# Kernel tuning notes

Measured on AMD Instinct MI355X. Metric: run time of the kernel, lower is better.

## Reference

```python
import jax, jax.numpy as jnp
import numpy as np

B, N, D, D1, R, O = 256, 32, 128, 128, 8, 8


def setup_inputs() -> dict:
    key = jax.random.key(0)
    k = jax.random.split(key, 7)
    return {
        "center_h": jax.random.normal(k[0], (B, D), dtype=jnp.float32),
        "raw_neighbors": jax.random.normal(k[1], (B, N, D), dtype=jnp.float32),
        "M": jax.random.normal(k[2], (R, O, D, D1), dtype=jnp.float32) * 0.05,
        "b": jax.random.normal(k[3], (R, O, D1), dtype=jnp.float32) * 0.01,
        "center_o": jax.random.randint(k[4], (B,), 0, O, dtype=jnp.int32),
        "s_types": jax.random.randint(k[5], (B, N), 0, R, dtype=jnp.int32),
        "o_types": jax.random.randint(k[6], (B, N), 0, O, dtype=jnp.int32),
    }


def reference(center_h, raw_neighbors, M, b, center_o, s_types, o_types):
    # --- center projection: for each example b, all relations r, with o = center_o[b]
    M_center = M[:, center_o]                      # [R, B, D, D1]
    b_center = b[:, center_o]                      # [R, B, D1]
    h_center = jnp.einsum('bd,rbdj->brj', center_h, M_center)  # [B, R, D1]
    h_center = h_center + jnp.transpose(b_center, (1, 0, 2))

    # --- neighbor projection: per-(example, neighbor) (s_type, o_type)-indexed matrix
    s_idx = jnp.maximum(s_types, 0)
    o_idx = jnp.maximum(o_types, 0)
    M_neighbor = M[s_idx, o_idx]                   # [B, N, D, D1] (large gather)
    h_neighbor = jnp.einsum('bnd,bndj->bnj', raw_neighbors, M_neighbor)  # [B, N, D1]
    h_neighbor = h_neighbor + b[s_idx, o_idx]

    # tf.nn.gelu default is exact (erf-based)
    return (jax.nn.gelu(h_center, approximate=False),
            jax.nn.gelu(h_neighbor, approximate=False))
```

## Files before the change

kernel.cpp:

```cpp
#include <hip/hip_runtime.h>
#include <math.h>

#define NPAIR 64
#define NCENTER 2048
#define WCAP 48
#define RSLOT 32

typedef __attribute__((ext_vector_type(8))) short bfrag8;
typedef __attribute__((ext_vector_type(8))) unsigned short u16x8;
typedef __attribute__((ext_vector_type(4))) float f32x4;

__device__ __forceinline__ float gelu_f(float v) {
    return 0.5f * v * (1.0f + erff(v * 0.70710678118654752f));
}
__device__ __forceinline__ unsigned short f2bf(float f) {
    unsigned int u = __float_as_uint(f);
    return (unsigned short)((u + 0x7FFFu + ((u >> 16) & 1u)) >> 16);
}

__global__ __launch_bounds__(256) void fused_kernel(
    const float* __restrict__ center_h,
    const float* __restrict__ raw_neighbors,
    const float* __restrict__ Mg,
    const float* __restrict__ bias,
    const int* __restrict__ center_o,
    const int* __restrict__ s_types,
    const int* __restrict__ o_types,
    float* __restrict__ out)
{
    __shared__ __align__(16) unsigned short Mbt[128 * 128];
    __shared__ __align__(16) unsigned short Xs[RSLOT * 128];
    __shared__ int list[4 * WCAP];
    __shared__ int cnts[4];
    __shared__ int rowid[RSLOT];

    const int t    = threadIdx.x;
    const int wave = t >> 6, lane = t & 63;
    const int pair = blockIdx.x & 63, slice = blockIdx.x >> 6;
    const int r0 = pair >> 3, o0 = pair & 7;

    const int4 svv = ((const int4*)s_types)[slice * 256 + t];
    const int4 ovv = ((const int4*)o_types)[slice * 256 + t];
    const int my_b  = slice * 32 + wave * 8 + (lane & 7);
    const int my_co = center_o[my_b];

    {
        const int dblk = t >> 4, cblk = t & 15;
        const float* bp = Mg + pair * 16384 + dblk * 8 * 128 + cblk * 8;
        float gg[8][8];
        #pragma unroll
        for (int r = 0; r < 8; ++r) {
            const float4 x0 = *(const float4*)(bp + r * 128);
            const float4 x1 = *(const float4*)(bp + r * 128 + 4);
            gg[r][0] = x0.x; gg[r][1] = x0.y; gg[r][2] = x0.z; gg[r][3] = x0.w;
            gg[r][4] = x1.x; gg[r][5] = x1.y; gg[r][6] = x1.z; gg[r][7] = x1.w;
        }
        #pragma unroll
        for (int i = 0; i < 8; ++i) {
            u16x8 w;
            #pragma unroll
            for (int j = 0; j < 8; ++j) w[j] = f2bf(gg[j][i]);
            const int c  = cblk * 8 + i;
            const int sl = (dblk ^ (cblk & 7) ^ i) << 4;
            *(u16x8*)((char*)Mbt + c * 256 + sl) = w;
        }
    }

    int cw = 0;
    {
        const bool match = (lane < 8) && (my_co == o0);
        const unsigned long long mk = __ballot(match);
        const int pre = __builtin_amdgcn_mbcnt_hi(
            (unsigned)(mk >> 32), __builtin_amdgcn_mbcnt_lo((unsigned)mk, 0));
        if (match) {
            const int pos = cw + pre;
            if (pos < WCAP) list[wave * WCAP + pos] = my_b * 8 + r0;
        }
        cw += __popcll(mk);
    }
    {
        const int ss[4] = { svv.x, svv.y, svv.z, svv.w };
        const int oo[4] = { ovv.x, ovv.y, ovv.z, ovv.w };
        const int base_nid = slice * 1024 + t * 4;
        #pragma unroll
        for (int j = 0; j < 4; ++j) {
            const int s = ss[j] < 0 ? 0 : ss[j];
            const int o = oo[j] < 0 ? 0 : oo[j];
            const bool match = (s == r0) & (o == o0);
            const unsigned long long mk = __ballot(match);
            const int pre = __builtin_amdgcn_mbcnt_hi(
                (unsigned)(mk >> 32), __builtin_amdgcn_mbcnt_lo((unsigned)mk, 0));
            if (match) {
                const int pos = cw + pre;
                if (pos < WCAP) list[wave * WCAP + pos] = NCENTER + base_nid + j;
            }
            cw += __popcll(mk);
            if (cw > WCAP) cw = WCAP;
        }
    }
    if (lane == 0) cnts[wave] = cw;
    __syncthreads();

    const int c0_ = cnts[0], c1_ = cnts[1], c2_ = cnts[2];
    const int cnt = c0_ + c1_ + c2_ + cnts[3];

    const int lo16 = lane & 15, hi4 = lane >> 4;
    const int cA = wave * 32 + lo16;
    const int cB = cA + 16;
    const float bvA = bias[pair * 128 + cA];
    const float bvB = bias[pair * 128 + cB];
    const int keyA = ((cA >> 3) & 7) ^ (cA & 7);
    const int keyB = ((cB >> 3) & 7) ^ (cB & 7);
    const int rsw  = lo16 & 7;

    for (int base = 0; base < cnt; base += RSLOT) {
        const int csz = (cnt - base < RSLOT) ? (cnt - base) : RSLOT;

        if (t < RSLOT) {
            int id = -1;
            int a = base + t;
            if (a < cnt) {
                int sw = 0;
                if (a >= c0_) { a -= c0_; sw = 1;
                    if (a >= c1_) { a -= c1_; sw = 2;
                        if (a >= c2_) { a -= c2_; sw = 3; } } }
                id = list[sw * WCAP + a];
            }
            rowid[t] = id;
        }
        __syncthreads();

        #pragma unroll
        for (int i = 0; i < 2; ++i) {
            const int flat = i * 256 + t;
            const int row = flat >> 4, ch = flat & 15;
            const int id = rowid[row];
            u16x8 w = {0, 0, 0, 0, 0, 0, 0, 0};
            if (id >= 0) {
                const float* xp = (id < NCENTER) ? center_h + (id >> 3) * 128
                                                 : raw_neighbors + (id - NCENTER) * 128;
                const float4 x0 = *(const float4*)(xp + ch * 8);
                const float4 x1 = *(const float4*)(xp + ch * 8 + 4);
                w[0] = f2bf(x0.x); w[1] = f2bf(x0.y); w[2] = f2bf(x0.z); w[3] = f2bf(x0.w);
                w[4] = f2bf(x1.x); w[5] = f2bf(x1.y); w[6] = f2bf(x1.z); w[7] = f2bf(x1.w);
            }
            *(u16x8*)((char*)Xs + row * 256 + ((ch ^ (row & 7)) << 4)) = w;
        }
        __syncthreads();

        f32x4 accA = {bvA, bvA, bvA, bvA};
        f32x4 accB = {bvB, bvB, bvB, bvB};
        f32x4 accC = accA, accD = accB;
        const int rowA = lo16, rowB = 16 + lo16;
        #pragma unroll
        for (int k = 0; k < 4; ++k) {
            const int dch = 4 * k + hi4;
            const bfrag8 aA = *(const bfrag8*)((const char*)Xs  + rowA * 256 + ((dch ^ rsw)  << 4));
            const bfrag8 aB = *(const bfrag8*)((const char*)Xs  + rowB * 256 + ((dch ^ rsw)  << 4));
            const bfrag8 b0 = *(const bfrag8*)((const char*)Mbt + cA   * 256 + ((dch ^ keyA) << 4));
            const bfrag8 b1 = *(const bfrag8*)((const char*)Mbt + cB   * 256 + ((dch ^ keyB) << 4));
            accA = __builtin_amdgcn_mfma_f32_16x16x32_bf16(aA, b0, accA, 0, 0, 0);
            accB = __builtin_amdgcn_mfma_f32_16x16x32_bf16(aA, b1, accB, 0, 0, 0);
            accC = __builtin_amdgcn_mfma_f32_16x16x32_bf16(aB, b0, accC, 0, 0, 0);
            accD = __builtin_amdgcn_mfma_f32_16x16x32_bf16(aB, b1, accD, 0, 0, 0);
        }

        #pragma unroll
        for (int j = 0; j < 4; ++j) {
            const int sA = hi4 * 4 + j;
            if (sA < csz) {
                const int gid = rowid[sA];
                out[gid * 128 + cA] = gelu_f(accA[j]);
                out[gid * 128 + cB] = gelu_f(accB[j]);
            }
            const int sB = 16 + hi4 * 4 + j;
            if (sB < csz) {
                const int gid = rowid[sB];
                out[gid * 128 + cA] = gelu_f(accC[j]);
                out[gid * 128 + cB] = gelu_f(accD[j]);
            }
        }
        __syncthreads();
    }
}

extern "C" void kernel_launch(void* const* d_in, const int* in_sizes, int n_in,
                              void* d_out, int out_size, void* d_ws, size_t ws_size,
                              hipStream_t stream) {
    const float* center_h      = (const float*)d_in[0];
    const float* raw_neighbors = (const float*)d_in[1];
    const float* M             = (const float*)d_in[2];
    const float* bias          = (const float*)d_in[3];
    const int*   center_o      = (const int*)d_in[4];
    const int*   s_types       = (const int*)d_in[5];
    const int*   o_types       = (const int*)d_in[6];
    float* out = (float*)d_out;

    fused_kernel<<<dim3(NPAIR * 8), dim3(256), 0, stream>>>(
        center_h, raw_neighbors, M, bias, center_o, s_types, o_types, out);
}
```

Baseline: 12.54 us.

## Split into bf16 pre-conversion kernel and MFMA kernel using direct global-to-LDS loads

Adds a conversion kernel that writes M (pre-swizzled, transposed) and all input rows as bf16 into workspace, so each of the 8 slice blocks per pair no longer re-reads and re-converts the fp32 weight matrix. The compute kernel then fills LDS with global_load_lds directly from the bf16 workspace, skipping register staging. This trades redundant conversion work and fp32 traffic for an extra kernel launch and a workspace round trip. It falls back to the fused kernel if the workspace is too small.

```diff
diff --git a/kernel.cpp b/kernel.cpp
--- a/kernel.cpp
+++ b/kernel.cpp
@@ -5,6 +5,10 @@
 #define NCENTER 2048
 #define WCAP 48
 #define RSLOT 32
+#define XROWS 8448
+#define WSM_BYTES (NPAIR * 32768)
+#define WSX_OFF   WSM_BYTES
+#define WS_NEED   (WSM_BYTES + XROWS * 256)
 
 typedef __attribute__((ext_vector_type(8))) short bfrag8;
 typedef __attribute__((ext_vector_type(8))) unsigned short u16x8;
@@ -16,6 +20,205 @@
 __device__ __forceinline__ unsigned short f2bf(float f) {
     unsigned int u = __float_as_uint(f);
     return (unsigned short)((u + 0x7FFFu + ((u >> 16) & 1u)) >> 16);
+}
+
+__global__ __launch_bounds__(256) void convert_kernel(
+    const float* __restrict__ center_h,
+    const float* __restrict__ raw_neighbors,
+    const float* __restrict__ Mg,
+    char* __restrict__ ws)
+{
+    const int t = threadIdx.x;
+    if (blockIdx.x < 256) {
+        const int pair = blockIdx.x >> 2, q = blockIdx.x & 3;
+        const int dblk = t >> 4;
+        const int cbase = q * 32 + (t & 15) * 2;
+        const float* bp = Mg + pair * 16384 + dblk * 8 * 128 + cbase;
+        float g0[8], g1[8];
+        #pragma unroll
+        for (int r = 0; r < 8; ++r) {
+            const float2 v = *(const float2*)(bp + r * 128);
+            g0[r] = v.x; g1[r] = v.y;
+        }
+        char* wm = ws + pair * 32768;
+        #pragma unroll
+        for (int cc = 0; cc < 2; ++cc) {
+            const int c = cbase + cc;
+            u16x8 w;
+            #pragma unroll
+            for (int j = 0; j < 8; ++j) w[j] = f2bf(cc ? g1[j] : g0[j]);
+            const int key = ((c >> 3) & 7) ^ (c & 7);
+            *(u16x8*)(wm + c * 256 + ((dblk ^ key) << 4)) = w;
+        }
+    } else {
+        const int xb = blockIdx.x - 256;
+        char* wx = ws + WSX_OFF;
+        for (int i = t; i < 33 * 16; i += 256) {
+            const int row = xb * 33 + (i >> 4);
+            const int ch = i & 15;
+            const float* src = (row < 256) ? center_h + row * 128
+                                           : raw_neighbors + (row - 256) * 128;
+            const float4 a = *(const float4*)(src + ch * 8);
+            const float4 b = *(const float4*)(src + ch * 8 + 4);
+            u16x8 w;
+            w[0] = f2bf(a.x); w[1] = f2bf(a.y); w[2] = f2bf(a.z); w[3] = f2bf(a.w);
+            w[4] = f2bf(b.x); w[5] = f2bf(b.y); w[6] = f2bf(b.z); w[7] = f2bf(b.w);
+            *(u16x8*)(wx + row * 256 + (ch << 4)) = w;
+        }
+    }
+}
+
+__global__ __launch_bounds__(256) void mfma_kernel(
+    const char* __restrict__ ws,
+    const float* __restrict__ bias,
+    const int* __restrict__ center_o,
+    const int* __restrict__ s_types,
+    const int* __restrict__ o_types,
+    float* __restrict__ out)
+{
+    __shared__ __align__(16) unsigned short Mbt[128 * 128];
+    __shared__ __align__(16) unsigned short Xs[RSLOT * 128];
+    __shared__ int list[4 * WCAP];
+    __shared__ int cnts[4];
+    __shared__ int rowid[RSLOT];
+
+    const int t    = threadIdx.x;
+    const int wave = t >> 6, lane = t & 63;
+    const int pair = blockIdx.x & 63, slice = blockIdx.x >> 6;
+    const int r0 = pair >> 3, o0 = pair & 7;
+
+    const int4 svv = ((const int4*)s_types)[slice * 256 + t];
+    const int4 ovv = ((const int4*)o_types)[slice * 256 + t];
+    const int my_b  = slice * 32 + wave * 8 + (lane & 7);
+    const int my_co = center_o[my_b];
+
+    {
+        const char* src = ws + pair * 32768;
+        #pragma unroll
+        for (int i = 0; i < 8; ++i) {
+            const int off = (i * 256 + t) * 16;
+            __builtin_amdgcn_global_load_lds(
+                (const __attribute__((address_space(1))) void*)(src + off),
+                (__attribute__((address_space(3))) void*)((char*)Mbt + off),
+                16, 0, 0);
+        }
+    }
+
+    int cw = 0;
+    {
+        const bool match = (lane < 8) && (my_co == o0);
+        const unsigned long long mk = __ballot(match);
+        const int pre = __builtin_amdgcn_mbcnt_hi(
+            (unsigned)(mk >> 32), __builtin_amdgcn_mbcnt_lo((unsigned)mk, 0));
+        if (match) {
+            const int pos = cw + pre;
+            if (pos < WCAP) list[wave * WCAP + pos] = my_b * 8 + r0;
+        }
+        cw += __popcll(mk);
+    }
+    {
+        const int ss[4] = { svv.x, svv.y, svv.z, svv.w };
+        const int oo[4] = { ovv.x, ovv.y, ovv.z, ovv.w };
+        const int base_nid = slice * 1024 + t * 4;
+        #pragma unroll
+        for (int j = 0; j < 4; ++j) {
+            const int s = ss[j] < 0 ? 0 : ss[j];
+            const int o = oo[j] < 0 ? 0 : oo[j];
+            const bool match = (s == r0) & (o == o0);
+            const unsigned long long mk = __ballot(match);
+            const int pre = __builtin_amdgcn_mbcnt_hi(
+                (unsigned)(mk >> 32), __builtin_amdgcn_mbcnt_lo((unsigned)mk, 0));
+            if (match) {
+                const int pos = cw + pre;
+                if (pos < WCAP) list[wave * WCAP + pos] = NCENTER + base_nid + j;
+            }
+            cw += __popcll(mk);
+            if (cw > WCAP) cw = WCAP;
+        }
+    }
+    if (lane == 0) cnts[wave] = cw;
+    __syncthreads();
+
+    const int c0_ = cnts[0], c1_ = cnts[1], c2_ = cnts[2];
+    const int cnt = c0_ + c1_ + c2_ + cnts[3];
+
+    const int lo16 = lane & 15, hi4 = lane >> 4;
+    const int cA = wave * 32 + lo16;
+    const int cB = cA + 16;
+    const float bvA = bias[pair * 128 + cA];
+    const float bvB = bias[pair * 128 + cB];
+    const int keyA = ((cA >> 3) & 7) ^ (cA & 7);
+    const int keyB = ((cB >> 3) & 7) ^ (cB & 7);
+    const int rsw  = lo16 & 7;
+    const char* wx = ws + WSX_OFF;
+
+    for (int base = 0; base < cnt; base += RSLOT) {
+        const int csz = (cnt - base < RSLOT) ? (cnt - base) : RSLOT;
+
+        if (t < RSLOT) {
+            int id = -1;
+            int a = base + t;
+            if (a < cnt) {
+                int sw = 0;
+                if (a >= c0_) { a -= c0_; sw = 1;
+                    if (a >= c1_) { a -= c1_; sw = 2;
+                        if (a >= c2_) { a -= c2_; sw = 3; } } }
+                id = list[sw * WCAP + a];
+            }
+            rowid[t] = id;
+        }
+        __syncthreads();
+
+        #pragma unroll
+        for (int i = 0; i < 2; ++i) {
+            const int flat = i * 256 + t;
+            const int slot = flat >> 4, ch = flat & 15;
+            const int id = rowid[slot];
+            if (id >= 0) {
+                const int xrow = (id < NCENTER) ? (id >> 3) : (256 + id - NCENTER);
+                const char* src = wx + xrow * 256 + ((ch ^ (slot & 7)) << 4);
+                __builtin_amdgcn_global_load_lds(
+                    (const __attribute__((address_space(1))) void*)src,
+                    (__attribute__((address_space(3))) void*)((char*)Xs + slot * 256 + (ch << 4)),
+                    16, 0, 0);
+            }
+        }
+        __syncthreads();
+
+        f32x4 accA = {bvA, bvA, bvA, bvA};
+        f32x4 accB = {bvB, bvB, bvB, bvB};
+        f32x4 accC = accA, accD = accB;
+        const int rowA = lo16, rowB = 16 + lo16;
+        #pragma unroll
+        for (int k = 0; k < 4; ++k) {
+            const int dch = 4 * k + hi4;
+            const bfrag8 aA = *(const bfrag8*)((const char*)Xs  + rowA * 256 + ((dch ^ rsw)  << 4));
+            const bfrag8 aB = *(const bfrag8*)((const char*)Xs  + rowB * 256 + ((dch ^ rsw)  << 4));
+            const bfrag8 b0 = *(const bfrag8*)((const char*)Mbt + cA   * 256 + ((dch ^ keyA) << 4));
+            const bfrag8 b1 = *(const bfrag8*)((const char*)Mbt + cB   * 256 + ((dch ^ keyB) << 4));
+            accA = __builtin_amdgcn_mfma_f32_16x16x32_bf16(aA, b0, accA, 0, 0, 0);
+            accB = __builtin_amdgcn_mfma_f32_16x16x32_bf16(aA, b1, accB, 0, 0, 0);
+            accC = __builtin_amdgcn_mfma_f32_16x16x32_bf16(aB, b0, accC, 0, 0, 0);
+            accD = __builtin_amdgcn_mfma_f32_16x16x32_bf16(aB, b1, accD, 0, 0, 0);
+        }
+
+        #pragma unroll
+        for (int j = 0; j < 4; ++j) {
+            const int sA = hi4 * 4 + j;
+            if (sA < csz) {
+                const int gid = rowid[sA];
+                out[gid * 128 + cA] = gelu_f(accA[j]);
+                out[gid * 128 + cB] = gelu_f(accB[j]);
+            }
+            const int sB = 16 + hi4 * 4 + j;
+            if (sB < csz) {
+                const int gid = rowid[sB];
+                out[gid * 128 + cA] = gelu_f(accC[j]);
+                out[gid * 128 + cB] = gelu_f(accD[j]);
+            }
+        }
+        __syncthreads();
+    }
 }
 
 __global__ __launch_bounds__(256) void fused_kernel(
@@ -196,6 +399,14 @@
     const int*   o_types       = (const int*)d_in[6];
     float* out = (float*)d_out;
 
-    fused_kernel<<<dim3(NPAIR * 8), dim3(256), 0, stream>>>(
-        center_h, raw_neighbors, M, bias, center_o, s_types, o_types, out);
-}
+    if (ws_size >= (size_t)WS_NEED) {
+        char* ws = (char*)d_ws;
+        convert_kernel<<<dim3(512), dim3(256), 0, stream>>>(
+            center_h, raw_neighbors, M, ws);
+        mfma_kernel<<<dim3(NPAIR * 8), dim3(256), 0, stream>>>(
+            ws, bias, center_o, s_types, o_types, out);
+    } else {
+        fused_kernel<<<dim3(NPAIR * 8), dim3(256), 0, stream>>>(
+            center_h, raw_neighbors, M, bias, center_o, s_types, o_types, out);
+    }
+}
```

New measurement: 17.09 us. 36.3% more time.

## Split output columns across two blocks per pair-slice to double grid parallelism

Applied to the files above, without the earlier changes.

Each block now handles half of the 128 output columns, so the grid doubles from 512 to 1024 blocks and each block stages only a 64x128 bf16 slice of the weight matrix in shared memory. The weight load is restructured into coalesced scalar loads issued before the type-matching scan, with the bf16 conversion and LDS store after it, so the global latency overlaps the ballot work. It also adds a launch-bounds occupancy hint and uses a single XOR swizzle for X and M. In exchange, the type scan and the gather of X rows are repeated in both column halves, and there are half as many MFMAs per wave.

```diff
diff --git a/kernel.cpp b/kernel.cpp
--- a/kernel.cpp
+++ b/kernel.cpp
@@ -18,7 +18,7 @@
     return (unsigned short)((u + 0x7FFFu + ((u >> 16) & 1u)) >> 16);
 }
 
-__global__ __launch_bounds__(256) void fused_kernel(
+__global__ __launch_bounds__(256, 4) void fused_kernel(
     const float* __restrict__ center_h,
     const float* __restrict__ raw_neighbors,
     const float* __restrict__ Mg,
@@ -28,7 +28,7 @@
     const int* __restrict__ o_types,
     float* __restrict__ out)
 {
-    __shared__ __align__(16) unsigned short Mbt[128 * 128];
+    __shared__ __align__(16) unsigned short Mbt[64 * 128];
     __shared__ __align__(16) unsigned short Xs[RSLOT * 128];
     __shared__ int list[4 * WCAP];
     __shared__ int cnts[4];
@@ -36,7 +36,10 @@
 
     const int t    = threadIdx.x;
     const int wave = t >> 6, lane = t & 63;
-    const int pair = blockIdx.x & 63, slice = blockIdx.x >> 6;
+    const int pair = blockIdx.x & 63;
+    const int rest = blockIdx.x >> 6;
+    const int ch   = rest & 1;
+    const int slice = rest >> 1;
     const int r0 = pair >> 3, o0 = pair & 7;
 
     const int4 svv = ((const int4*)s_types)[slice * 256 + t];
@@ -44,26 +47,15 @@
     const int my_b  = slice * 32 + wave * 8 + (lane & 7);
     const int my_co = center_o[my_b];
 
+    const int lane16 = t & 15, dblk = t >> 4;
+    float g[4][8];
     {
-        const int dblk = t >> 4, cblk = t & 15;
-        const float* bp = Mg + pair * 16384 + dblk * 8 * 128 + cblk * 8;
-        float gg[8][8];
+        const float* mp = Mg + pair * 16384 + (dblk * 8) * 128 + ch * 64;
         #pragma unroll
-        for (int r = 0; r < 8; ++r) {
-            const float4 x0 = *(const float4*)(bp + r * 128);
-            const float4 x1 = *(const float4*)(bp + r * 128 + 4);
-            gg[r][0] = x0.x; gg[r][1] = x0.y; gg[r][2] = x0.z; gg[r][3] = x0.w;
-            gg[r][4] = x1.x; gg[r][5] = x1.y; gg[r][6] = x1.z; gg[r][7] = x1.w;
-        }
-        #pragma unroll
-        for (int i = 0; i < 8; ++i) {
-            u16x8 w;
+        for (int i = 0; i < 4; ++i)
             #pragma unroll
-            for (int j = 0; j < 8; ++j) w[j] = f2bf(gg[j][i]);
-            const int c  = cblk * 8 + i;
-            const int sl = (dblk ^ (cblk & 7) ^ i) << 4;
-            *(u16x8*)((char*)Mbt + c * 256 + sl) = w;
-        }
+            for (int r = 0; r < 8; ++r)
+                g[i][r] = mp[r * 128 + 16 * i + lane16];
     }
 
     int cw = 0;
@@ -99,19 +91,24 @@
         }
     }
     if (lane == 0) cnts[wave] = cw;
+
+    #pragma unroll
+    for (int i = 0; i < 4; ++i) {
+        const int c = 16 * i + lane16;
+        u16x8 w;
+        #pragma unroll
+        for (int r = 0; r < 8; ++r) w[r] = f2bf(g[i][r]);
+        *(u16x8*)((char*)Mbt + c * 256 + ((dblk ^ lane16) << 4)) = w;
+    }
     __syncthreads();
 
     const int c0_ = cnts[0], c1_ = cnts[1], c2_ = cnts[2];
     const int cnt = c0_ + c1_ + c2_ + cnts[3];
 
     const int lo16 = lane & 15, hi4 = lane >> 4;
-    const int cA = wave * 32 + lo16;
-    const int cB = cA + 16;
-    const float bvA = bias[pair * 128 + cA];
-    const float bvB = bias[pair * 128 + cB];
-    const int keyA = ((cA >> 3) & 7) ^ (cA & 7);
-    const int keyB = ((cB >> 3) & 7) ^ (cB & 7);
-    const int rsw  = lo16 & 7;
+    const int c_loc = wave * 16 + lo16;
+    const int colg  = ch * 64 + c_loc;
+    const float bv = bias[pair * 128 + colg];
 
     for (int base = 0; base < cnt; base += RSLOT) {
         const int csz = (cnt - base < RSLOT) ? (cnt - base) : RSLOT;
@@ -133,52 +130,40 @@
         #pragma unroll
         for (int i = 0; i < 2; ++i) {
             const int flat = i * 256 + t;
-            const int row = flat >> 4, ch = flat & 15;
-            const int id = rowid[row];
+            const int slot = flat >> 4, chg = flat & 15;
+            const int id = rowid[slot];
             u16x8 w = {0, 0, 0, 0, 0, 0, 0, 0};
             if (id >= 0) {
                 const float* xp = (id < NCENTER) ? center_h + (id >> 3) * 128
                                                  : raw_neighbors + (id - NCENTER) * 128;
-                const float4 x0 = *(const float4*)(xp + ch * 8);
-                const float4 x1 = *(const float4*)(xp + ch * 8 + 4);
+                const float4 x0 = *(const float4*)(xp + chg * 8);
+                const float4 x1 = *(const float4*)(xp + chg * 8 + 4);
                 w[0] = f2bf(x0.x); w[1] = f2bf(x0.y); w[2] = f2bf(x0.z); w[3] = f2bf(x0.w);
                 w[4] = f2bf(x1.x); w[5] = f2bf(x1.y); w[6] = f2bf(x1.z); w[7] = f2bf(x1.w);
             }
-            *(u16x8*)((char*)Xs + row * 256 + ((ch ^ (row & 7)) << 4)) = w;
+            *(u16x8*)((char*)Xs + slot * 256 + ((chg ^ (slot & 15)) << 4)) = w;
         }
         __syncthreads();
 
-        f32x4 accA = {bvA, bvA, bvA, bvA};
-        f32x4 accB = {bvB, bvB, bvB, bvB};
-        f32x4 accC = accA, accD = accB;
-        const int rowA = lo16, rowB = 16 + lo16;
+        f32x4 accA = {bv, bv, bv, bv};
+        f32x4 accC = accA;
         #pragma unroll
         for (int k = 0; k < 4; ++k) {
             const int dch = 4 * k + hi4;
-            const bfrag8 aA = *(const bfrag8*)((const char*)Xs  + rowA * 256 + ((dch ^ rsw)  << 4));
-            const bfrag8 aB = *(const bfrag8*)((const char*)Xs  + rowB * 256 + ((dch ^ rsw)  << 4));
-            const bfrag8 b0 = *(const bfrag8*)((const char*)Mbt + cA   * 256 + ((dch ^ keyA) << 4));
-            const bfrag8 b1 = *(const bfrag8*)((const char*)Mbt + cB   * 256 + ((dch ^ keyB) << 4));
+            const int gsl = (dch ^ lo16) << 4;
+            const bfrag8 aA = *(const bfrag8*)((const char*)Xs  + lo16 * 256 + gsl);
+            const bfrag8 aB = *(const bfrag8*)((const char*)Xs  + (16 + lo16) * 256 + gsl);
+            const bfrag8 b0 = *(const bfrag8*)((const char*)Mbt + c_loc * 256 + gsl);
             accA = __builtin_amdgcn_mfma_f32_16x16x32_bf16(aA, b0, accA, 0, 0, 0);
-            accB = __builtin_amdgcn_mfma_f32_16x16x32_bf16(aA, b1, accB, 0, 0, 0);
             accC = __builtin_amdgcn_mfma_f32_16x16x32_bf16(aB, b0, accC, 0, 0, 0);
-            accD = __builtin_amdgcn_mfma_f32_16x16x32_bf16(aB, b1, accD, 0, 0, 0);
         }
 
         #pragma unroll
         for (int j = 0; j < 4; ++j) {
             const int sA = hi4 * 4 + j;
-            if (sA < csz) {
-                const int gid = rowid[sA];
-                out[gid * 128 + cA] = gelu_f(accA[j]);
-                out[gid * 128 + cB] = gelu_f(accB[j]);
-            }
+            if (sA < csz) out[rowid[sA] * 128 + colg] = gelu_f(accA[j]);
             const int sB = 16 + hi4 * 4 + j;
-            if (sB < csz) {
-                const int gid = rowid[sB];
-                out[gid * 128 + cA] = gelu_f(accC[j]);
-                out[gid * 128 + cB] = gelu_f(accD[j]);
-            }
+            if (sB < csz) out[rowid[sB] * 128 + colg] = gelu_f(accC[j]);
         }
         __syncthreads();
     }
@@ -196,6 +181,6 @@
     const int*   o_types       = (const int*)d_in[6];
     float* out = (float*)d_out;
 
-    fused_kernel<<<dim3(NPAIR * 8), dim3(256), 0, stream>>>(
+    fused_kernel<<<dim3(NPAIR * 16), dim3(256), 0, stream>>>(
         center_h, raw_neighbors, M, bias, center_o, s_types, o_types, out);
 }
```

New measurement: 11.91 us (median of 2 runs). -5.0%, faster.
